# Performance work log

Measured on AMD Instinct MI355X. Metric: run time of the kernel, lower is better.

## Reference

```python
import jax, jax.numpy as jnp
import numpy as np

B, D, R = 256, 4096, 8
MAX_R = 2 * R - 1  # static upper bound on radius (torch uses data-dependent max)


def setup_inputs() -> dict:
    key = jax.random.key(0)
    ks = jax.random.split(key, 6)
    x = jax.random.randint(ks[0], (B, D), 0, 2).astype(jnp.float32)  # binary spins
    W = jax.random.normal(ks[1], (D, D), jnp.float32) / np.float32(np.sqrt(D))
    b = jax.random.normal(ks[2], (D,), jnp.float32)
    radius_raw = jax.random.randint(ks[3], (B, 1), 0, MAX_R)  # +1 in reference -> [1, 2R-1]
    gumbel_u = jax.random.uniform(ks[4], (B, D), jnp.float32)
    u = jax.random.uniform(ks[5], (B,), jnp.float32)
    return {"x": x, "W": W, "b": b, "radius_raw": radius_raw, "gumbel_u": gumbel_u, "u": u}


def _model(x, W, b):
    # quadratic pseudo-Boolean energy model: per-sample scalar score
    return 0.5 * jnp.einsum('bi,ij,bj->b', x, W, x) + x @ b


def reference(x, W, b, radius_raw, gumbel_u, u):
    radius = radius_raw + 1                                   # [B,1] in [1, 2R-1]
    r_mask = (jnp.arange(MAX_R)[None, :] < radius).astype(x.dtype)  # [B, MAX_R]

    score_x = _model(x, W, b)                                 # [B]
    grad = jax.lax.stop_gradient(
        jax.grad(lambda xx: _model(xx, W, b).sum())(x))       # [B,D], detached

    delta_x = -(2.0 * x - 1.0)
    score_change_x = delta_x * grad / 2.0                     # logits of proposal

    # multinomial without replacement == Gumbel top-k on the logits
    eps = 1e-10
    g = -jnp.log(-jnp.log(jnp.clip(gumbel_u, eps, 1.0 - eps)))
    _, indices = jax.lax.top_k(score_change_x + g, MAX_R)     # [B, MAX_R]

    rows = jnp.arange(B)[:, None]
    cur_bits = x[rows, indices]                               # gather
    new_bits = 1.0 - cur_bits
    y = x.at[rows, indices].set(r_mask * new_bits + (1.0 - r_mask) * cur_bits)

    delta_y = -(2.0 * y - 1.0)
    score_y = _model(y, W, b)
    score_change_y = delta_y * grad / 2.0

    log_pypx = score_y - score_x
    log_tilde_pxpy = -jnp.sum(grad * (y - x), axis=-1)
    log_zxzy = (jax.scipy.special.logsumexp(score_change_x, axis=-1)
                - jax.scipy.special.logsumexp(score_change_y, axis=-1))
    log_acc = jnp.minimum(log_pypx + log_tilde_pxpy + log_zxzy, 0.0)

    accepted = (jnp.exp(log_acc) > u).astype(x.dtype)[:, None]  # [B,1]
    return y * accepted + (1.0 - accepted) * x
```

## Files before the change

kernel.cpp:

```cpp
#include <hip/hip_runtime.h>

#define Bsz 256
#define Dd  4096
#define MAXR 15
#define FMAX 3.402823466e+38f
#define BK 64
#define LSTRIDE 72

typedef short bf16x8 __attribute__((ext_vector_type(8)));
typedef float f32x4  __attribute__((ext_vector_type(4)));

__device__ __forceinline__ unsigned short f2bf(float f) {
    unsigned int u = __float_as_uint(f);
    unsigned int r = (u + 0x7fffu + ((u >> 16) & 1u)) >> 16;
    return (unsigned short)r;
}
__device__ __forceinline__ float bf2f(unsigned short h) {
    return __uint_as_float(((unsigned int)h) << 16);
}

__global__ __launch_bounds__(256) void k_ssym(const float* __restrict__ W,
                                              const float* __restrict__ x,
                                              unsigned short* __restrict__ shi,
                                              unsigned short* __restrict__ slo,
                                              unsigned short* __restrict__ xb) {
    __shared__ float t1[64][68];
    __shared__ float t2[64][68];
    int bid = blockIdx.x;
    int bi = 0;
    while (bid >= 64 - bi) { bid -= 64 - bi; ++bi; }
    const int bj = bi + bid;
    const int i0 = bi * 64, j0 = bj * 64;
    const int tid = threadIdx.x;

    #pragma unroll
    for (int sb = 0; sb < 4; ++sb) {
        int s = sb * 256 + tid;
        int r = s >> 4, q = (s & 15) * 4;
        *(float4*)&t1[r][q] = *(const float4*)(W + (size_t)(i0 + r) * Dd + j0 + q);
        *(float4*)&t2[r][q] = *(const float4*)(W + (size_t)(j0 + r) * Dd + i0 + q);
    }
    __syncthreads();

    const int r = tid >> 2, c0 = (tid & 3) * 16;
    {
        unsigned short vh[16], vl[16];
        #pragma unroll
        for (int k = 0; k < 16; ++k) {
            float s = 0.5f * (t1[r][c0 + k] + t2[c0 + k][r]);
            vh[k] = f2bf(s);
            vl[k] = f2bf(s - bf2f(vh[k]));
        }
        size_t o = (size_t)(i0 + r) * Dd + j0 + c0;
        *(uint4*)(shi + o) = *(const uint4*)&vh[0];
        *(uint4*)(shi + o + 8) = *(const uint4*)&vh[8];
        *(uint4*)(slo + o) = *(const uint4*)&vl[0];
        *(uint4*)(slo + o + 8) = *(const uint4*)&vl[8];
    }
    if (bi != bj) {
        unsigned short vh[16], vl[16];
        #pragma unroll
        for (int k = 0; k < 16; ++k) {
            float s = 0.5f * (t2[r][c0 + k] + t1[c0 + k][r]);
            vh[k] = f2bf(s);
            vl[k] = f2bf(s - bf2f(vh[k]));
        }
        size_t o = (size_t)(j0 + r) * Dd + i0 + c0;
        *(uint4*)(shi + o) = *(const uint4*)&vh[0];
        *(uint4*)(shi + o + 8) = *(const uint4*)&vh[8];
        *(uint4*)(slo + o) = *(const uint4*)&vl[0];
        *(uint4*)(slo + o + 8) = *(const uint4*)&vl[8];
    }

    if (blockIdx.x < 256) {
        const float* xp = x + (size_t)blockIdx.x * 4096;
        unsigned short* xo = xb + (size_t)blockIdx.x * 4096;
        #pragma unroll
        for (int c = 0; c < 4; ++c) {
            int e = c * 1024 + tid * 4;
            float4 v = *(const float4*)(xp + e);
            unsigned short o4[4] = { f2bf(v.x), f2bf(v.y), f2bf(v.z), f2bf(v.w) };
            *(uint2*)(xo + e) = *(const uint2*)o4;
        }
    }
}

__global__ __launch_bounds__(512, 2) void k_gemm(const unsigned short* __restrict__ xb,
                                              const unsigned short* __restrict__ shi,
                                              const unsigned short* __restrict__ slo,
                                              float* __restrict__ part,
                                              int kchunk) {
    __shared__ __align__(16) unsigned short As[256 * LSTRIDE];
    __shared__ __align__(16) unsigned short Bh[64 * LSTRIDE];
    __shared__ __align__(16) unsigned short Bl[64 * LSTRIDE];
    const int tid = threadIdx.x;
    const int n0 = blockIdx.x * 64;
    const int kbase = blockIdx.z * kchunk;
    const int w = tid >> 6, lane = tid & 63;
    const int ln = lane & 15, quad = lane >> 4;
    const int wm = w >> 1, wn = w & 1;

    unsigned ga[4]; int la[4];
    #pragma unroll
    for (int j = 0; j < 4; ++j) {
        int s = tid + j * 512;
        int r = s >> 3, g = s & 7;
        ga[j] = (unsigned)(r * Dd + kbase + g * 8);
        la[j] = r * LSTRIDE + g * 8;
    }
    const int rb2 = tid >> 3, gb2 = tid & 7;
    const unsigned gb = (unsigned)((n0 + rb2) * Dd + kbase + gb2 * 8);
    const int lb = rb2 * LSTRIDE + gb2 * 8;

    f32x4 acc[4][2];
    #pragma unroll
    for (int mt = 0; mt < 4; ++mt)
        #pragma unroll
        for (int ct = 0; ct < 2; ++ct)
            #pragma unroll
            for (int rr = 0; rr < 4; ++rr) acc[mt][ct][rr] = 0.0f;

    bf16x8 va[4], vh, vl;
    #pragma unroll
    for (int j = 0; j < 4; ++j) va[j] = *(const bf16x8*)(xb + ga[j]);
    vh = *(const bf16x8*)(shi + gb);
    vl = *(const bf16x8*)(slo + gb);

    for (int k0 = 0; k0 < kchunk; k0 += BK) {
        __syncthreads();
        #pragma unroll
        for (int j = 0; j < 4; ++j) *(bf16x8*)&As[la[j]] = va[j];
        *(bf16x8*)&Bh[lb] = vh;
        *(bf16x8*)&Bl[lb] = vl;
        {
            int kn = k0 + BK;
            int ks = (kn < kchunk) ? kn : 0;
            #pragma unroll
            for (int j = 0; j < 4; ++j) va[j] = *(const bf16x8*)(xb + ga[j] + ks);
            vh = *(const bf16x8*)(shi + gb + ks);
            vl = *(const bf16x8*)(slo + gb + ks);
        }
        __syncthreads();
        #pragma unroll
        for (int kk = 0; kk < BK; kk += 32) {
            const int gr = (kk >> 3) + quad;
            bf16x8 a[4];
            #pragma unroll
            for (int mt = 0; mt < 4; ++mt)
                a[mt] = *(const bf16x8*)&As[(wm * 64 + mt * 16 + ln) * LSTRIDE + gr * 8];
            #pragma unroll
            for (int ct = 0; ct < 2; ++ct) {
                int rb = wn * 32 + ct * 16 + ln;
                bf16x8 bh = *(const bf16x8*)&Bh[rb * LSTRIDE + gr * 8];
                bf16x8 bl = *(const bf16x8*)&Bl[rb * LSTRIDE + gr * 8];
                #pragma unroll
                for (int mt = 0; mt < 4; ++mt) {
                    acc[mt][ct] = __builtin_amdgcn_mfma_f32_16x16x32_bf16(a[mt], bh, acc[mt][ct], 0, 0, 0);
                    acc[mt][ct] = __builtin_amdgcn_mfma_f32_16x16x32_bf16(a[mt], bl, acc[mt][ct], 0, 0, 0);
                }
            }
        }
    }
    float* prow = part + (size_t)blockIdx.z * (Bsz * Dd);
    #pragma unroll
    for (int mt = 0; mt < 4; ++mt)
        #pragma unroll
        for (int ct = 0; ct < 2; ++ct)
            #pragma unroll
            for (int rr = 0; rr < 4; ++rr) {
                int m = wm * 64 + mt * 16 + quad * 4 + rr;
                int n = n0 + wn * 32 + ct * 16 + ln;
                prow[(size_t)m * Dd + n] = acc[mt][ct][rr];
            }
}

__device__ __forceinline__ float block_max256(float v, float* redf) {
    #pragma unroll
    for (int off = 32; off; off >>= 1) v = fmaxf(v, __shfl_down(v, off));
    __syncthreads();
    if ((threadIdx.x & 63) == 0) redf[threadIdx.x >> 6] = v;
    __syncthreads();
    return fmaxf(fmaxf(redf[0], redf[1]), fmaxf(redf[2], redf[3]));
}
__device__ __forceinline__ float block_sum256(float v, float* redf) {
    #pragma unroll
    for (int off = 32; off; off >>= 1) v += __shfl_down(v, off);
    __syncthreads();
    if ((threadIdx.x & 63) == 0) redf[threadIdx.x >> 6] = v;
    __syncthreads();
    return (redf[0] + redf[1]) + (redf[2] + redf[3]);
}

__global__ __launch_bounds__(256, 1) void k_epilogue(const float* __restrict__ x,
                                                  const float* __restrict__ W,
                                                  const int* __restrict__ radius_raw,
                                                  const float* __restrict__ gu,
                                                  const float* __restrict__ uvec,
                                                  const float* __restrict__ part,
                                                  const float* __restrict__ bias,
                                                  float* __restrict__ out,
                                                  int nsplit) {
    __shared__ float scx_s[Dd];
    __shared__ float redf[2][4];
    __shared__ int   redi[2][4];
    __shared__ float redsum[4];
    __shared__ int   flips[MAXR];

    const int b = blockIdx.x;
    const int tid = threadIdx.x;
    const float* xrow  = x  + (size_t)b * Dd;
    const float* gurow = gu + (size_t)b * Dd;

    float4 g4[4], bs4[4], xv4[4], uu4[4];
    #pragma unroll
    for (int c = 0; c < 4; ++c) {
        int j = c * 1024 + tid * 4;
        g4[c]  = *(const float4*)(part + (size_t)b * Dd + j);
        bs4[c] = *(const float4*)(bias + j);
        xv4[c] = *(const float4*)(xrow + j);
        uu4[c] = *(const float4*)(gurow + j);
    }
    if (nsplit == 4) {
        float4 p1[4], p2[4], p3[4];
        #pragma unroll
        for (int c = 0; c < 4; ++c) {
            int j = c * 1024 + tid * 4;
            p1[c] = *(const float4*)(part + (size_t)(1 * Bsz + b) * Dd + j);
            p2[c] = *(const float4*)(part + (size_t)(2 * Bsz + b) * Dd + j);
            p3[c] = *(const float4*)(part + (size_t)(3 * Bsz + b) * Dd + j);
        }
        #pragma unroll
        for (int c = 0; c < 4; ++c) {
            g4[c].x = ((g4[c].x + p1[c].x) + p2[c].x) + p3[c].x;
            g4[c].y = ((g4[c].y + p1[c].y) + p2[c].y) + p3[c].y;
            g4[c].z = ((g4[c].z + p1[c].z) + p2[c].z) + p3[c].z;
            g4[c].w = ((g4[c].w + p1[c].w) + p2[c].w) + p3[c].w;
        }
    } else {
        for (int z = 1; z < nsplit; ++z) {
            const float* pz = part + (size_t)z * (Bsz * Dd) + (size_t)b * Dd;
            #pragma unroll
            for (int c = 0; c < 4; ++c) {
                float4 a = *(const float4*)(pz + c * 1024 + tid * 4);
                g4[c].x += a.x; g4[c].y += a.y; g4[c].z += a.z; g4[c].w += a.w;
            }
        }
    }
    float sc[16], ky[16];
    float lmax = -FMAX;
    float lkey = -FMAX; int lidx = 0x7fffffff;
    #pragma unroll
    for (int c = 0; c < 4; ++c) {
        const float* gg = (const float*)&g4[c];
        const float* gc = (const float*)&bs4[c];
        const float* gx = (const float*)&xv4[c];
        const float* gup = (const float*)&uu4[c];
        #pragma unroll
        for (int e = 0; e < 4; ++e) {
            int r = c * 4 + e;
            float g = gg[e] + gc[e];
            float s = (1.0f - 2.0f * gx[e]) * g * 0.5f;
            float k = s - logf(-logf(fmaxf(gup[e], 1e-10f)));
            sc[r] = s;
            ky[r] = k;
            lmax = fmaxf(lmax, s);
            if (k > lkey) { lkey = k; lidx = c * 1024 + tid * 4 + e; }
        }
        *(float4*)&scx_s[c * 1024 + tid * 4] = *(const float4*)&sc[c * 4];
    }

    float mx = block_max256(lmax, redsum);
    float ls = 0.0f;
    #pragma unroll
    for (int r = 0; r < 16; ++r) ls += expf(sc[r] - mx);
    float sum_x = block_sum256(ls, redsum);
    float lse_x = mx + logf(sum_x);

    const int radius = radius_raw[b] + 1;
    unsigned removed = 0;
    for (int t = 0; t < radius; ++t) {
        float v = lkey; int idx = lidx;
        #pragma unroll
        for (int off = 32; off; off >>= 1) {
            float v2 = __shfl_down(v, off);
            int   i2 = __shfl_down(idx, off);
            if (v2 > v || (v2 == v && i2 < idx)) { v = v2; idx = i2; }
        }
        const int buf = t & 1;
        if ((tid & 63) == 0) { redf[buf][tid >> 6] = v; redi[buf][tid >> 6] = idx; }
        __syncthreads();
        float bv = redf[buf][0]; int bi = redi[buf][0];
        #pragma unroll
        for (int w2 = 1; w2 < 4; ++w2) {
            float v2 = redf[buf][w2]; int i2 = redi[buf][w2];
            if (v2 > bv || (v2 == bv && i2 < bi)) { bv = v2; bi = i2; }
        }
        if (tid == ((bi >> 2) & 255)) {
            removed |= 1u << (((bi >> 10) << 2) | (bi & 3));
            lkey = -FMAX; lidx = 0x7fffffff;
            #pragma unroll
            for (int c = 0; c < 4; ++c)
                #pragma unroll
                for (int e = 0; e < 4; ++e) {
                    int r = c * 4 + e;
                    if (!(removed & (1u << r)) && ky[r] > lkey) {
                        lkey = ky[r]; lidx = c * 1024 + tid * 4 + e;
                    }
                }
        }
        if (tid == 0) flips[t] = bi;
    }
    __syncthreads();

    float delta = 0.0f;
    if (tid < radius) {
        float sv = scx_s[flips[tid]];
        delta = expf(-sv - mx) - expf(sv - mx);
    }
    float sum_y = sum_x + block_sum256(delta, redsum);
    float lse_y = mx + logf(sum_y);

    float ts = 0.0f;
    for (int t = tid; t < radius * radius; t += 256) {
        int p = flips[t / radius], q = flips[t % radius];
        float dp = 1.0f - 2.0f * xrow[p];
        float dq = 1.0f - 2.0f * xrow[q];
        ts += 0.25f * dp * dq * (W[(size_t)p * Dd + q] + W[(size_t)q * Dd + p]);
    }
    float T = block_sum256(ts, redsum);

    float log_acc = fminf(T + lse_x - lse_y, 0.0f);
    int accepted = (expf(log_acc) > uvec[b]) ? 1 : 0;

    float* orow = out + (size_t)b * Dd;
    #pragma unroll
    for (int c = 0; c < 4; ++c)
        *(float4*)(orow + c * 1024 + tid * 4) = xv4[c];
    __syncthreads();
    if (accepted && tid < radius) {
        int p = flips[tid];
        orow[p] = 1.0f - xrow[p];
    }
}

extern "C" void kernel_launch(void* const* d_in, const int* in_sizes, int n_in,
                              void* d_out, int out_size, void* d_ws, size_t ws_size,
                              hipStream_t stream) {
    const float* x          = (const float*)d_in[0];
    const float* W          = (const float*)d_in[1];
    const float* bias       = (const float*)d_in[2];
    const int*   radius_raw = (const int*)d_in[3];
    const float* gu         = (const float*)d_in[4];
    const float* u          = (const float*)d_in[5];
    float* out = (float*)d_out;

    unsigned short* shi = (unsigned short*)d_ws;
    unsigned short* slo = shi + (size_t)Dd * Dd;
    unsigned short* xb  = slo + (size_t)Dd * Dd;
    float*          prt = (float*)(xb + (size_t)Bsz * Dd);

    const size_t fixed = (size_t)2 * Dd * Dd * 2 + (size_t)Bsz * Dd * 2;
    const int nsplit = (ws_size >= fixed + (size_t)4 * Bsz * Dd * 4) ? 4 : 2;
    const int kchunk = Dd / nsplit;

    k_ssym<<<2080, 256, 0, stream>>>(W, x, shi, slo, xb);
    k_gemm<<<dim3(64, 1, nsplit), 512, 0, stream>>>(xb, shi, slo, prt, kchunk);
    k_epilogue<<<Bsz, 256, 0, stream>>>(x, W, radius_raw, gu, u, prt, bias, out, nsplit);
}
```

Measured before the change: 168.5 us.

## Fuse W symmetrization and bf16 hi/lo split into GEMM tile loading

Removes the separate symmetrize kernel that wrote the bf16 hi and lo copies of (W+W^T)/2. The GEMM now loads fp32 W tiles for both orientations, transposes one through shared memory, and builds the hi/lo split on the fly. The x operand is read directly from global memory instead of being staged in LDS. This drops a full D×D write-then-read round trip, at the cost of reading fp32 W twice per tile, an extra sync, and uncached global A-fragment loads.

```diff
diff --git a/kernel.cpp b/kernel.cpp
--- a/kernel.cpp
+++ b/kernel.cpp
@@ -19,80 +19,28 @@
     return __uint_as_float(((unsigned int)h) << 16);
 }
 
-__global__ __launch_bounds__(256) void k_ssym(const float* __restrict__ W,
-                                              const float* __restrict__ x,
-                                              unsigned short* __restrict__ shi,
-                                              unsigned short* __restrict__ slo,
-                                              unsigned short* __restrict__ xb) {
-    __shared__ float t1[64][68];
-    __shared__ float t2[64][68];
-    int bid = blockIdx.x;
-    int bi = 0;
-    while (bid >= 64 - bi) { bid -= 64 - bi; ++bi; }
-    const int bj = bi + bid;
-    const int i0 = bi * 64, j0 = bj * 64;
+__global__ __launch_bounds__(256) void k_xconv(const float* __restrict__ x,
+                                               unsigned short* __restrict__ xb) {
+    const int b = blockIdx.x;
     const int tid = threadIdx.x;
-
-    #pragma unroll
-    for (int sb = 0; sb < 4; ++sb) {
-        int s = sb * 256 + tid;
-        int r = s >> 4, q = (s & 15) * 4;
-        *(float4*)&t1[r][q] = *(const float4*)(W + (size_t)(i0 + r) * Dd + j0 + q);
-        *(float4*)&t2[r][q] = *(const float4*)(W + (size_t)(j0 + r) * Dd + i0 + q);
-    }
-    __syncthreads();
-
-    const int r = tid >> 2, c0 = (tid & 3) * 16;
-    {
-        unsigned short vh[16], vl[16];
-        #pragma unroll
-        for (int k = 0; k < 16; ++k) {
-            float s = 0.5f * (t1[r][c0 + k] + t2[c0 + k][r]);
-            vh[k] = f2bf(s);
-            vl[k] = f2bf(s - bf2f(vh[k]));
-        }
-        size_t o = (size_t)(i0 + r) * Dd + j0 + c0;
-        *(uint4*)(shi + o) = *(const uint4*)&vh[0];
-        *(uint4*)(shi + o + 8) = *(const uint4*)&vh[8];
-        *(uint4*)(slo + o) = *(const uint4*)&vl[0];
-        *(uint4*)(slo + o + 8) = *(const uint4*)&vl[8];
-    }
-    if (bi != bj) {
-        unsigned short vh[16], vl[16];
-        #pragma unroll
-        for (int k = 0; k < 16; ++k) {
-            float s = 0.5f * (t2[r][c0 + k] + t1[c0 + k][r]);
-            vh[k] = f2bf(s);
-            vl[k] = f2bf(s - bf2f(vh[k]));
-        }
-        size_t o = (size_t)(j0 + r) * Dd + i0 + c0;
-        *(uint4*)(shi + o) = *(const uint4*)&vh[0];
-        *(uint4*)(shi + o + 8) = *(const uint4*)&vh[8];
-        *(uint4*)(slo + o) = *(const uint4*)&vl[0];
-        *(uint4*)(slo + o + 8) = *(const uint4*)&vl[8];
-    }
-
-    if (blockIdx.x < 256) {
-        const float* xp = x + (size_t)blockIdx.x * 4096;
-        unsigned short* xo = xb + (size_t)blockIdx.x * 4096;
-        #pragma unroll
-        for (int c = 0; c < 4; ++c) {
-            int e = c * 1024 + tid * 4;
-            float4 v = *(const float4*)(xp + e);
-            unsigned short o4[4] = { f2bf(v.x), f2bf(v.y), f2bf(v.z), f2bf(v.w) };
-            *(uint2*)(xo + e) = *(const uint2*)o4;
-        }
+    const float* xp = x + (size_t)b * Dd;
+    unsigned short* xo = xb + (size_t)b * Dd;
+    #pragma unroll
+    for (int c = 0; c < 4; ++c) {
+        int e = c * 1024 + tid * 4;
+        float4 v = *(const float4*)(xp + e);
+        unsigned short o4[4] = { f2bf(v.x), f2bf(v.y), f2bf(v.z), f2bf(v.w) };
+        *(uint2*)(xo + e) = *(const uint2*)o4;
     }
 }
 
 __global__ __launch_bounds__(512, 2) void k_gemm(const unsigned short* __restrict__ xb,
-                                              const unsigned short* __restrict__ shi,
-                                              const unsigned short* __restrict__ slo,
+                                              const float* __restrict__ W,
                                               float* __restrict__ part,
                                               int kchunk) {
-    __shared__ __align__(16) unsigned short As[256 * LSTRIDE];
     __shared__ __align__(16) unsigned short Bh[64 * LSTRIDE];
     __shared__ __align__(16) unsigned short Bl[64 * LSTRIDE];
+    __shared__ __align__(8)  float T1[64 * 66];
     const int tid = threadIdx.x;
     const int n0 = blockIdx.x * 64;
     const int kbase = blockIdx.z * kchunk;
@@ -100,17 +48,15 @@
     const int ln = lane & 15, quad = lane >> 4;
     const int wm = w >> 1, wn = w & 1;
 
-    unsigned ga[4]; int la[4];
-    #pragma unroll
-    for (int j = 0; j < 4; ++j) {
-        int s = tid + j * 512;
-        int r = s >> 3, g = s & 7;
-        ga[j] = (unsigned)(r * Dd + kbase + g * 8);
-        la[j] = r * LSTRIDE + g * 8;
-    }
-    const int rb2 = tid >> 3, gb2 = tid & 7;
-    const unsigned gb = (unsigned)((n0 + rb2) * Dd + kbase + gb2 * 8);
-    const int lb = rb2 * LSTRIDE + gb2 * 8;
+    const int rT = tid >> 3;
+    const int cT8 = (tid & 7) * 8;
+    const float* w1p = W + (size_t)(kbase + rT) * Dd + (n0 + cT8);
+    const float* w2p = W + (size_t)(n0 + rT) * Dd + (kbase + cT8);
+
+    const unsigned short* xA[4];
+    #pragma unroll
+    for (int mt = 0; mt < 4; ++mt)
+        xA[mt] = xb + (size_t)(wm * 64 + mt * 16 + ln) * Dd + kbase;
 
     f32x4 acc[4][2];
     #pragma unroll
@@ -120,25 +66,45 @@
             #pragma unroll
             for (int rr = 0; rr < 4; ++rr) acc[mt][ct][rr] = 0.0f;
 
-    bf16x8 va[4], vh, vl;
-    #pragma unroll
-    for (int j = 0; j < 4; ++j) va[j] = *(const bf16x8*)(xb + ga[j]);
-    vh = *(const bf16x8*)(shi + gb);
-    vl = *(const bf16x8*)(slo + gb);
+    float4 w1a = *(const float4*)(w1p);
+    float4 w1b = *(const float4*)(w1p + 4);
+    float4 w2a = *(const float4*)(w2p);
+    float4 w2b = *(const float4*)(w2p + 4);
 
     for (int k0 = 0; k0 < kchunk; k0 += BK) {
         __syncthreads();
-        #pragma unroll
-        for (int j = 0; j < 4; ++j) *(bf16x8*)&As[la[j]] = va[j];
-        *(bf16x8*)&Bh[lb] = vh;
-        *(bf16x8*)&Bl[lb] = vl;
         {
-            int kn = k0 + BK;
-            int ks = (kn < kchunk) ? kn : 0;
-            #pragma unroll
-            for (int j = 0; j < 4; ++j) va[j] = *(const bf16x8*)(xb + ga[j] + ks);
-            vh = *(const bf16x8*)(shi + gb + ks);
-            vl = *(const bf16x8*)(slo + gb + ks);
+            float2 p0 = { w1a.x, w1a.y }, p1 = { w1a.z, w1a.w };
+            float2 p2 = { w1b.x, w1b.y }, p3 = { w1b.z, w1b.w };
+            float* t = &T1[rT * 66 + cT8];
+            *(float2*)(t + 0) = p0; *(float2*)(t + 2) = p1;
+            *(float2*)(t + 4) = p2; *(float2*)(t + 6) = p3;
+        }
+        int kn = k0 + BK;
+        int ks = (kn < kchunk) ? kn : 0;
+        float4 nw1a = *(const float4*)(w1p + (size_t)ks * Dd);
+        float4 nw1b = *(const float4*)(w1p + (size_t)ks * Dd + 4);
+        float4 nw2a = *(const float4*)(w2p + ks);
+        float4 nw2b = *(const float4*)(w2p + ks + 4);
+        __syncthreads();
+        {
+            const float* w2f = (const float*)&w2a;
+            float sv[8];
+            #pragma unroll
+            for (int j = 0; j < 4; ++j)
+                sv[j] = 0.5f * (w2f[j] + T1[(cT8 + j) * 66 + rT]);
+            const float* w2g = (const float*)&w2b;
+            #pragma unroll
+            for (int j = 0; j < 4; ++j)
+                sv[4 + j] = 0.5f * (w2g[j] + T1[(cT8 + 4 + j) * 66 + rT]);
+            unsigned short vh[8], vl[8];
+            #pragma unroll
+            for (int j = 0; j < 8; ++j) {
+                vh[j] = f2bf(sv[j]);
+                vl[j] = f2bf(sv[j] - bf2f(vh[j]));
+            }
+            *(bf16x8*)&Bh[rT * LSTRIDE + cT8] = *(const bf16x8*)&vh[0];
+            *(bf16x8*)&Bl[rT * LSTRIDE + cT8] = *(const bf16x8*)&vl[0];
         }
         __syncthreads();
         #pragma unroll
@@ -147,7 +113,7 @@
             bf16x8 a[4];
             #pragma unroll
             for (int mt = 0; mt < 4; ++mt)
-                a[mt] = *(const bf16x8*)&As[(wm * 64 + mt * 16 + ln) * LSTRIDE + gr * 8];
+                a[mt] = *(const bf16x8*)(xA[mt] + k0 + gr * 8);
             #pragma unroll
             for (int ct = 0; ct < 2; ++ct) {
                 int rb = wn * 32 + ct * 16 + ln;
@@ -160,6 +126,7 @@
                 }
             }
         }
+        w1a = nw1a; w1b = nw1b; w2a = nw2a; w2b = nw2b;
     }
     float* prow = part + (size_t)blockIdx.z * (Bsz * Dd);
     #pragma unroll
@@ -354,16 +321,14 @@
     const float* u          = (const float*)d_in[5];
     float* out = (float*)d_out;
 
-    unsigned short* shi = (unsigned short*)d_ws;
-    unsigned short* slo = shi + (size_t)Dd * Dd;
-    unsigned short* xb  = slo + (size_t)Dd * Dd;
+    unsigned short* xb  = (unsigned short*)d_ws;
     float*          prt = (float*)(xb + (size_t)Bsz * Dd);
 
-    const size_t fixed = (size_t)2 * Dd * Dd * 2 + (size_t)Bsz * Dd * 2;
+    const size_t fixed = (size_t)Bsz * Dd * 2;
     const int nsplit = (ws_size >= fixed + (size_t)4 * Bsz * Dd * 4) ? 4 : 2;
     const int kchunk = Dd / nsplit;
 
-    k_ssym<<<2080, 256, 0, stream>>>(W, x, shi, slo, xb);
-    k_gemm<<<dim3(64, 1, nsplit), 512, 0, stream>>>(xb, shi, slo, prt, kchunk);
+    k_xconv<<<Bsz, 256, 0, stream>>>(x, xb);
+    k_gemm<<<dim3(64, 1, nsplit), 512, 0, stream>>>(xb, W, prt, kchunk);
     k_epilogue<<<Bsz, 256, 0, stream>>>(x, W, radius_raw, gu, u, prt, bias, out, nsplit);
 }
```

Measured after the change: 173.4 us. +2.9%, slower.

## Double-buffer LDS tiles in GEMM to drop one barrier per k-step

Applied to the files above, without the earlier changes.

Converts the GEMM's shared-memory A/B tiles into two ping-pong buffers. Each iteration writes the next tile into the alternate buffer while computing on the current one, which leaves a single __syncthreads per k-step instead of two. This doubles LDS usage (~55KB per block), which may reduce occupancy below the 2 blocks/CU requested by launch bounds.

```diff
diff --git a/kernel.cpp b/kernel.cpp
--- a/kernel.cpp
+++ b/kernel.cpp
@@ -90,9 +90,9 @@
                                               const unsigned short* __restrict__ slo,
                                               float* __restrict__ part,
                                               int kchunk) {
-    __shared__ __align__(16) unsigned short As[256 * LSTRIDE];
-    __shared__ __align__(16) unsigned short Bh[64 * LSTRIDE];
-    __shared__ __align__(16) unsigned short Bl[64 * LSTRIDE];
+    __shared__ __align__(16) unsigned short As[2][256 * LSTRIDE];
+    __shared__ __align__(16) unsigned short Bh[2][64 * LSTRIDE];
+    __shared__ __align__(16) unsigned short Bl[2][64 * LSTRIDE];
     const int tid = threadIdx.x;
     const int n0 = blockIdx.x * 64;
     const int kbase = blockIdx.z * kchunk;
@@ -120,39 +120,55 @@
             #pragma unroll
             for (int rr = 0; rr < 4; ++rr) acc[mt][ct][rr] = 0.0f;
 
+    const int nst = kchunk / BK;
+
     bf16x8 va[4], vh, vl;
     #pragma unroll
-    for (int j = 0; j < 4; ++j) va[j] = *(const bf16x8*)(xb + ga[j]);
+    for (int j = 0; j < 4; ++j) va[j] = *(const bf16x8*)(xb  + ga[j]);
     vh = *(const bf16x8*)(shi + gb);
     vl = *(const bf16x8*)(slo + gb);
-
-    for (int k0 = 0; k0 < kchunk; k0 += BK) {
+    #pragma unroll
+    for (int j = 0; j < 4; ++j) *(bf16x8*)&As[0][la[j]] = va[j];
+    *(bf16x8*)&Bh[0][lb] = vh;
+    *(bf16x8*)&Bl[0][lb] = vl;
+    {
+        int ks = (nst > 1) ? BK : 0;
+        #pragma unroll
+        for (int j = 0; j < 4; ++j) va[j] = *(const bf16x8*)(xb  + ga[j] + ks);
+        vh = *(const bf16x8*)(shi + gb + ks);
+        vl = *(const bf16x8*)(slo + gb + ks);
+    }
+
+    for (int t = 0; t < nst; ++t) {
+        const int cur = t & 1;
         __syncthreads();
         #pragma unroll
-        for (int j = 0; j < 4; ++j) *(bf16x8*)&As[la[j]] = va[j];
-        *(bf16x8*)&Bh[lb] = vh;
-        *(bf16x8*)&Bl[lb] = vl;
+        for (int j = 0; j < 4; ++j) *(bf16x8*)&As[cur ^ 1][la[j]] = va[j];
+        *(bf16x8*)&Bh[cur ^ 1][lb] = vh;
+        *(bf16x8*)&Bl[cur ^ 1][lb] = vl;
         {
-            int kn = k0 + BK;
+            int kn = (t + 2) * BK;
             int ks = (kn < kchunk) ? kn : 0;
             #pragma unroll
-            for (int j = 0; j < 4; ++j) va[j] = *(const bf16x8*)(xb + ga[j] + ks);
+            for (int j = 0; j < 4; ++j) va[j] = *(const bf16x8*)(xb  + ga[j] + ks);
             vh = *(const bf16x8*)(shi + gb + ks);
             vl = *(const bf16x8*)(slo + gb + ks);
         }
-        __syncthreads();
+        const unsigned short* Ar = As[cur];
+        const unsigned short* Hr = Bh[cur];
+        const unsigned short* Lr = Bl[cur];
         #pragma unroll
         for (int kk = 0; kk < BK; kk += 32) {
             const int gr = (kk >> 3) + quad;
             bf16x8 a[4];
             #pragma unroll
             for (int mt = 0; mt < 4; ++mt)
-                a[mt] = *(const bf16x8*)&As[(wm * 64 + mt * 16 + ln) * LSTRIDE + gr * 8];
+                a[mt] = *(const bf16x8*)&Ar[(wm * 64 + mt * 16 + ln) * LSTRIDE + gr * 8];
             #pragma unroll
             for (int ct = 0; ct < 2; ++ct) {
                 int rb = wn * 32 + ct * 16 + ln;
-                bf16x8 bh = *(const bf16x8*)&Bh[rb * LSTRIDE + gr * 8];
-                bf16x8 bl = *(const bf16x8*)&Bl[rb * LSTRIDE + gr * 8];
+                bf16x8 bh = *(const bf16x8*)&Hr[rb * LSTRIDE + gr * 8];
+                bf16x8 bl = *(const bf16x8*)&Lr[rb * LSTRIDE + gr * 8];
                 #pragma unroll
                 for (int mt = 0; mt < 4; ++mt) {
                     acc[mt][ct] = __builtin_amdgcn_mfma_f32_16x16x32_bf16(a[mt], bh, acc[mt][ct], 0, 0, 0);
```

Result: no change. 166.6 us (median of 2 runs) (-1.1%).

## Use direct global-to-LDS loads with double-buffered swizzled shared tiles in GEMM

Applied to the files above, without the earlier changes.

Replaces the register-staged copy of the A and B tiles into padded shared memory with global_load_lds direct-to-LDS loads into two shared buffers. An XOR swizzle replaces the padding to avoid bank conflicts. This removes the VGPR round trip and one barrier per K step, and lets the next tile load while the current one is computed. It doubles LDS use, which may lower occupancy. The vmcnt(0) wait at the top of each iteration limits how much load latency is hidden.

```diff
diff --git a/kernel.cpp b/kernel.cpp
--- a/kernel.cpp
+++ b/kernel.cpp
@@ -5,7 +5,6 @@
 #define MAXR 15
 #define FMAX 3.402823466e+38f
 #define BK 64
-#define LSTRIDE 72
 
 typedef short bf16x8 __attribute__((ext_vector_type(8)));
 typedef float f32x4  __attribute__((ext_vector_type(4)));
@@ -18,6 +17,10 @@
 __device__ __forceinline__ float bf2f(unsigned short h) {
     return __uint_as_float(((unsigned int)h) << 16);
 }
+
+#define GLOAD16(gp, lp) __builtin_amdgcn_global_load_lds(                     \
+    (const __attribute__((address_space(1))) void*)(gp),                      \
+    (__attribute__((address_space(3))) void*)(lp), 16, 0, 0)
 
 __global__ __launch_bounds__(256) void k_ssym(const float* __restrict__ W,
                                               const float* __restrict__ x,
@@ -90,9 +93,9 @@
                                               const unsigned short* __restrict__ slo,
                                               float* __restrict__ part,
                                               int kchunk) {
-    __shared__ __align__(16) unsigned short As[256 * LSTRIDE];
-    __shared__ __align__(16) unsigned short Bh[64 * LSTRIDE];
-    __shared__ __align__(16) unsigned short Bl[64 * LSTRIDE];
+    __shared__ __align__(16) unsigned short As[2][256 * 64];
+    __shared__ __align__(16) unsigned short Bh[2][64 * 64];
+    __shared__ __align__(16) unsigned short Bl[2][64 * 64];
     const int tid = threadIdx.x;
     const int n0 = blockIdx.x * 64;
     const int kbase = blockIdx.z * kchunk;
@@ -100,17 +103,8 @@
     const int ln = lane & 15, quad = lane >> 4;
     const int wm = w >> 1, wn = w & 1;
 
-    unsigned ga[4]; int la[4];
-    #pragma unroll
-    for (int j = 0; j < 4; ++j) {
-        int s = tid + j * 512;
-        int r = s >> 3, g = s & 7;
-        ga[j] = (unsigned)(r * Dd + kbase + g * 8);
-        la[j] = r * LSTRIDE + g * 8;
-    }
-    const int rb2 = tid >> 3, gb2 = tid & 7;
-    const unsigned gb = (unsigned)((n0 + rb2) * Dd + kbase + gb2 * 8);
-    const int lb = rb2 * LSTRIDE + gb2 * 8;
+    const int sw = ((((lane & 7) * 16) ^ ((lane >> 3) * 16)) >> 1);
+    const int rsl = lane >> 3;
 
     f32x4 acc[4][2];
     #pragma unroll
@@ -120,39 +114,43 @@
             #pragma unroll
             for (int rr = 0; rr < 4; ++rr) acc[mt][ct][rr] = 0.0f;
 
-    bf16x8 va[4], vh, vl;
-    #pragma unroll
-    for (int j = 0; j < 4; ++j) va[j] = *(const bf16x8*)(xb + ga[j]);
-    vh = *(const bf16x8*)(shi + gb);
-    vl = *(const bf16x8*)(slo + gb);
-
-    for (int k0 = 0; k0 < kchunk; k0 += BK) {
+    const int nst = kchunk / BK;
+
+    auto stage = [&](int sel, int kt) {
+        #pragma unroll
+        for (int j = 0; j < 4; ++j) {
+            int ch = w * 4 + j;
+            int row = ch * 8 + rsl;
+            GLOAD16(xb + (size_t)row * Dd + kbase + kt + sw, &As[sel][ch * 512]);
+        }
+        int brow = w * 8 + rsl;
+        GLOAD16(shi + (size_t)(n0 + brow) * Dd + kbase + kt + sw, &Bh[sel][w * 512]);
+        GLOAD16(slo + (size_t)(n0 + brow) * Dd + kbase + kt + sw, &Bl[sel][w * 512]);
+    };
+
+    stage(0, 0);
+
+    for (int t = 0; t < nst; ++t) {
+        const int cur = t & 1;
+        asm volatile("s_waitcnt vmcnt(0)" ::: "memory");
         __syncthreads();
-        #pragma unroll
-        for (int j = 0; j < 4; ++j) *(bf16x8*)&As[la[j]] = va[j];
-        *(bf16x8*)&Bh[lb] = vh;
-        *(bf16x8*)&Bl[lb] = vl;
-        {
-            int kn = k0 + BK;
-            int ks = (kn < kchunk) ? kn : 0;
-            #pragma unroll
-            for (int j = 0; j < 4; ++j) va[j] = *(const bf16x8*)(xb + ga[j] + ks);
-            vh = *(const bf16x8*)(shi + gb + ks);
-            vl = *(const bf16x8*)(slo + gb + ks);
-        }
-        __syncthreads();
+        if (t + 1 < nst) stage(cur ^ 1, (t + 1) * BK);
+        const unsigned short* Ar = As[cur];
+        const unsigned short* Hr = Bh[cur];
+        const unsigned short* Lr = Bl[cur];
         #pragma unroll
         for (int kk = 0; kk < BK; kk += 32) {
             const int gr = (kk >> 3) + quad;
+            const int sx = (gr * 8) ^ ((ln & 7) * 8);
             bf16x8 a[4];
             #pragma unroll
             for (int mt = 0; mt < 4; ++mt)
-                a[mt] = *(const bf16x8*)&As[(wm * 64 + mt * 16 + ln) * LSTRIDE + gr * 8];
+                a[mt] = *(const bf16x8*)&Ar[(wm * 64 + mt * 16 + ln) * 64 + sx];
             #pragma unroll
             for (int ct = 0; ct < 2; ++ct) {
                 int rb = wn * 32 + ct * 16 + ln;
-                bf16x8 bh = *(const bf16x8*)&Bh[rb * LSTRIDE + gr * 8];
-                bf16x8 bl = *(const bf16x8*)&Bl[rb * LSTRIDE + gr * 8];
+                bf16x8 bh = *(const bf16x8*)&Hr[rb * 64 + sx];
+                bf16x8 bl = *(const bf16x8*)&Lr[rb * 64 + sx];
                 #pragma unroll
                 for (int mt = 0; mt < 4; ++mt) {
                     acc[mt][ct] = __builtin_amdgcn_mfma_f32_16x16x32_bf16(a[mt], bh, acc[mt][ct], 0, 0, 0);
```

After: 170.3 us. Within noise of the previous version (+1.1%).
